# Optimization experiments

Hardware: AMD Instinct MI355X
Metric: run time of the kernel (lower is better)

Reference implementation:

```python
import jax, jax.numpy as jnp
import numpy as np

B = 2048      # batch
IN = 784      # input_dim (28*28, hardcoded by x.view(-1,28,28))
H = 512       # hidden_dim
OUT = 512     # output_dim
E = 8         # n_experts
ER = 4        # n_recurrent (experts 0..3 are LSTM experts)
ES = E - ER   # simple MLP experts
T = 28        # LSTM timesteps
F = 28        # LSTM input features per step
K = 5         # n_active = max(1, int(8*0.7))
TEMP = 2.718281828459045  # np.e


def setup_inputs() -> dict:
    key = jax.random.key(0)
    ks = jax.random.split(key, 14)
    s = 0.05
    return {
        "x":    jax.random.normal(ks[0], (B, IN), dtype=jnp.float32),
        # Boltzmann gate
        "Wg":   jax.random.normal(ks[1], (E, IN), dtype=jnp.float32) * s,
        "bg":   jnp.zeros((E,), dtype=jnp.float32),
        # Recurrent experts (stacked over ER): PyTorch LSTM layout, gate order i,f,g,o
        "Wih":  jax.random.normal(ks[2], (ER, 4 * H, F), dtype=jnp.float32) * s,
        "Whh":  jax.random.normal(ks[3], (ER, 4 * H, H), dtype=jnp.float32) * s,
        "bih":  jnp.zeros((ER, 4 * H), dtype=jnp.float32),
        "bhh":  jnp.zeros((ER, 4 * H), dtype=jnp.float32),
        "fcW":  jax.random.normal(ks[4], (ER, OUT, H), dtype=jnp.float32) * s,
        "fcb":  jnp.zeros((ER, OUT), dtype=jnp.float32),
        # Simple experts (stacked over ES)
        "W1":   jax.random.normal(ks[5], (ES, H, IN), dtype=jnp.float32) * s,
        "b1":   jnp.zeros((ES, H), dtype=jnp.float32),
        "W2":   jax.random.normal(ks[6], (ES, OUT, H), dtype=jnp.float32) * s,
        "b2":   jnp.zeros((ES, OUT), dtype=jnp.float32),
    }


def _forward(x, Wg, bg, Wih, Whh, bih, bhh, fcW, fcb, W1, b1, W2, b2):
    # --- Boltzmann gate: softmax(scores/T), top-k mask, renormalize ---
    scores = (x @ Wg.T + bg) / TEMP                    # [B,E]
    probs = jax.nn.softmax(scores, axis=-1)
    _, idx = jax.lax.top_k(probs, K)                   # [B,K]
    mask = jax.nn.one_hot(idx, E, dtype=probs.dtype).sum(axis=-2)  # [B,E]
    w = probs * mask
    weights = w / (w.sum(axis=-1, keepdims=True) + 1e-8)

    # --- Recurrent experts (vectorized over ER, scan over time) ---
    xs = x.reshape(B, T, F)
    xs_t = jnp.transpose(xs, (1, 0, 2))                # [T,B,F]

    def step(carry, x_t):
        h, c = carry                                   # each [ER,B,H]
        gates = (jnp.einsum('bi,egi->ebg', x_t, Wih) + bih[:, None, :]
                 + jnp.einsum('ebh,egh->ebg', h, Whh) + bhh[:, None, :])  # [ER,B,4H]
        i_g = jax.nn.sigmoid(gates[..., 0 * H:1 * H])
        f_g = jax.nn.sigmoid(gates[..., 1 * H:2 * H])
        g_g = jnp.tanh(gates[..., 2 * H:3 * H])
        o_g = jax.nn.sigmoid(gates[..., 3 * H:4 * H])
        c = f_g * c + i_g * g_g
        h = o_g * jnp.tanh(c)
        return (h, c), None

    h0 = jnp.zeros((ER, B, H), dtype=x.dtype)
    (h_last, _), _ = jax.lax.scan(step, (h0, h0), xs_t)
    rec_out = jnp.einsum('ebh,eoh->ebo', h_last, fcW) + fcb[:, None, :]   # [ER,B,OUT]

    # --- Simple experts (dropout is identity at eval) ---
    h1 = jax.nn.relu(jnp.einsum('bi,ehi->ebh', x, W1) + b1[:, None, :])   # [ES,B,H]
    simp_out = jnp.einsum('ebh,eoh->ebo', h1, W2) + b2[:, None, :]        # [ES,B,OUT]

    expert_outputs = jnp.concatenate([rec_out, simp_out], axis=0)         # [E,B,OUT]
    return jnp.einsum('be,ebo->bo', weights, expert_outputs)              # [B,OUT]


def reference(x, Wg, bg, Wih, Whh, bih, bhh, fcW, fcb, W1, b1, W2, b2):
    return _forward(x, Wg, bg, Wih, Whh, bih, bhh, fcW, fcb, W1, b1, W2, b2)
```

## Files before the change

### kernel.cpp

```cpp
#include <hip/hip_runtime.h>
#include <stdint.h>

#define CDIV(a,b) (((a)+(b)-1)/(b))

typedef unsigned short u16;
using bf16x8   = __attribute__((ext_vector_type(8))) short;
using floatx4  = __attribute__((ext_vector_type(4))) float;
using floatx16 = __attribute__((ext_vector_type(16))) float;

constexpr int B_N   = 2048;
constexpr int IN_N  = 784;
constexpr int H_N   = 512;
constexpr int OUT_N = 512;
constexpr int E_N   = 8;
constexpr int ER_N  = 4;
constexpr int ES_N  = 4;
constexpr int T_N   = 28;
constexpr int F_N   = 28;
constexpr int G4H   = 2048;
constexpr int KA    = 544;
constexpr int KB8   = KA / 8;
constexpr int NKI   = KA / 16;
constexpr int XP    = 800;

__device__ __forceinline__ u16 f2bf(float f) {
  union { float f; uint32_t u; } v; v.f = f;
  uint32_t r = v.u + 0x7fffu + ((v.u >> 16) & 1u);
  return (u16)(r >> 16);
}
__device__ __forceinline__ float sigm(float x) {
  return __builtin_amdgcn_rcpf(1.f + __expf(-x));
}
__device__ __forceinline__ float tanhf_(float x) {
  return __builtin_fmaf(-2.f, __builtin_amdgcn_rcpf(__expf(2.f * x) + 1.f), 1.f);
}

__device__ __forceinline__ void async16(const void* g, void* l) {
  __builtin_amdgcn_global_load_lds(
      (__attribute__((address_space(1))) void*)g,
      (__attribute__((address_space(3))) void*)l, 16, 0, 0);
}

__global__ __launch_bounds__(1024, 4)
void lstm_persist(const u16* __restrict__ Wc, const float* __restrict__ brec,
                  const u16* __restrict__ xb, u16* __restrict__ A0,
                  u16* __restrict__ A1, u16* __restrict__ Hlast,
                  int* __restrict__ Gbar)
{
  extern __shared__ __align__(16) u16 Ws[];
  const int tid  = threadIdx.x;
  const int lane = tid & 63;
  const int wave = tid >> 6;
  const int blk  = blockIdx.x;
  const int xcd  = blk & 7;
  const int i8   = blk >> 3;
  const int nt   = i8 & 15;
  const int g    = (i8 >> 4) * 8 + xcd;
  const int z    = g >> 2;
  const int mr   = g & 3;
  const int ln   = lane & 31;
  const int hw   = lane >> 5;
  const int gslot = g * 64;

  {
    const u16* Wsrc = Wc + (size_t)(z * 16 + nt) * (4 * KB8 * 256);
    for (int off = tid * 8; off < 4 * KB8 * 256; off += 1024 * 8)
      async16(Wsrc + off, Ws + off);
  }

  float bb[4];
#pragma unroll
  for (int j = 0; j < 4; ++j)
    bb[j] = brec[((z * 16 + nt) * 4 + j) * 32 + ln];

  float c[16];
#pragma unroll
  for (int r = 0; r < 16; ++r) c[r] = 0.f;

  const int mblk = mr * 16 + wave;
  const int hcol = nt * 32 + ln;
  const size_t zoff = (size_t)z * ((size_t)64 * KB8 * 256);
  __syncthreads();

  for (int t = 0; t < T_N; ++t) {
    const u16* Az  = ((t & 1) ? A1 : A0) + zoff;
    u16*       Aoz = ((t & 1) ? A0 : A1) + zoff;

    const u16* Ap = Az + ((size_t)mblk * KB8 + hw) * 256 + ln * 8;

    bf16x8 pa[2];
    pa[0] = *(const bf16x8*)Ap;
    pa[1] = *(const bf16x8*)(Ap + 512);

    floatx16 acc[4];
#pragma unroll
    for (int j = 0; j < 4; ++j)
#pragma unroll
      for (int r = 0; r < 16; ++r)
        acc[j][r] = bb[j];

#pragma unroll 2
    for (int kk = 0; kk < NKI; ++kk) {
      bf16x8 a = pa[kk & 1];
      if (kk + 2 < NKI)
        pa[kk & 1] = *(const bf16x8*)(Ap + (size_t)(kk + 2) * 512);
      const u16* Bp = Ws + (2 * kk + hw) * 256 + ln * 8;
      bf16x8 b0 = *(const bf16x8*)(Bp);
      bf16x8 b1 = *(const bf16x8*)(Bp + 1 * KB8 * 256);
      bf16x8 b2 = *(const bf16x8*)(Bp + 2 * KB8 * 256);
      bf16x8 b3 = *(const bf16x8*)(Bp + 3 * KB8 * 256);
      acc[0] = __builtin_amdgcn_mfma_f32_32x32x16_bf16(a, b0, acc[0], 0, 0, 0);
      acc[1] = __builtin_amdgcn_mfma_f32_32x32x16_bf16(a, b1, acc[1], 0, 0, 0);
      acc[2] = __builtin_amdgcn_mfma_f32_32x32x16_bf16(a, b2, acc[2], 0, 0, 0);
      acc[3] = __builtin_amdgcn_mfma_f32_32x32x16_bf16(a, b3, acc[3], 0, 0, 0);
    }

    const int last = (t == T_N - 1);
#pragma unroll
    for (int r = 0; r < 16; ++r) {
      float cv = sigm(acc[1][r]) * c[r] + sigm(acc[0][r]) * tanhf_(acc[2][r]);
      c[r] = cv;
      u16 hb = f2bf(sigm(acc[3][r]) * tanhf_(cv));
      int mrow = 4 * hw + (r & 3) + 8 * (r >> 2);
      if (!last)
        __builtin_nontemporal_store(hb,
            &Aoz[((size_t)mblk * KB8 + (hcol >> 3)) * 256 + mrow * 8 + (hcol & 7)]);
      else
        Hlast[((size_t)(z * B_N + mblk * 32 + mrow)) * H_N + hcol] = hb;
    }

    if (t + 1 < T_N) {
      for (int idx = nt * 1024 + tid; idx < 512 * F_N; idx += 16 * 1024) {
        int ml  = idx / F_N, col = idx - ml * F_N;
        int m   = mr * 512 + ml;
        int k   = H_N + col;
        __builtin_nontemporal_store(xb[(size_t)m * XP + (t + 1) * F_N + col],
            &Aoz[((size_t)(m >> 5) * KB8 + (k >> 3)) * 256 + (m & 31) * 8 + (k & 7)]);
      }

      __syncthreads();
      if (tid == 0) {
        __hip_atomic_fetch_add(&Gbar[gslot], 1, __ATOMIC_RELEASE,
                               __HIP_MEMORY_SCOPE_AGENT);
        const int target = 16 * (t + 1);
        while (__hip_atomic_load(&Gbar[gslot], __ATOMIC_RELAXED,
                                 __HIP_MEMORY_SCOPE_AGENT) < target)
          __builtin_amdgcn_s_sleep(1);
        __builtin_amdgcn_fence(__ATOMIC_ACQUIRE, "agent");
      }
      __syncthreads();
    }
  }
}

template<int RELU, int OBF>
__global__ __launch_bounds__(256, 2)
void gemm_bt(const u16* __restrict__ A, int lda, long sAz,
             const u16* __restrict__ Bw, int ldb, long sBz,
             const float* __restrict__ bias, int sBiz,
             void* __restrict__ Cv, int ldc, long sCz,
             int K)
{
  __shared__ __align__(16) u16 As[128 * 32];
  __shared__ __align__(16) u16 Bs[128 * 32];
  const int tid  = threadIdx.x;
  const int lane = tid & 63;
  const int wave = tid >> 6;
  const int m0 = blockIdx.y * 128;
  const int n0 = blockIdx.x * 128;
  const int z  = blockIdx.z;
  const u16* Ab = A  + (size_t)z * sAz;
  const u16* Bb = Bw + (size_t)z * sBz;

  const int wm   = (wave & 1) * 64;
  const int wn   = (wave >> 1) * 64;
  const int lm   = lane & 15;
  const int quad = lane >> 4;

  const int s0 = wave * 64 + lane;
  const int r0 = s0 >> 2, c0 = (s0 & 3) * 8;
  const int s1 = s0 + 256;
  const int r1 = s1 >> 2, c1 = (s1 & 3) * 8;

  floatx4 acc[4][4] = {};

  for (int k0 = 0; k0 < K; k0 += 32) {
    async16(Ab + (size_t)(m0 + r0) * lda + (k0 + c0), As + wave * 512);
    async16(Ab + (size_t)(m0 + r1) * lda + (k0 + c1), As + 2048 + wave * 512);
    async16(Bb + (size_t)(n0 + r0) * ldb + (k0 + c0), Bs + wave * 512);
    async16(Bb + (size_t)(n0 + r1) * ldb + (k0 + c1), Bs + 2048 + wave * 512);
    __syncthreads();
    bf16x8 af[4], bf_[4];
#pragma unroll
    for (int i = 0; i < 4; ++i)
      af[i] = *(const bf16x8*)&As[(wm + i * 16 + lm) * 32 + quad * 8];
#pragma unroll
    for (int j = 0; j < 4; ++j)
      bf_[j] = *(const bf16x8*)&Bs[(wn + j * 16 + lm) * 32 + quad * 8];
#pragma unroll
    for (int i = 0; i < 4; ++i)
#pragma unroll
      for (int j = 0; j < 4; ++j)
        acc[i][j] = __builtin_amdgcn_mfma_f32_16x16x32_bf16(af[i], bf_[j], acc[i][j], 0, 0, 0);
    __syncthreads();
  }

  float bj[4];
#pragma unroll
  for (int j = 0; j < 4; ++j)
    bj[j] = bias ? bias[z * sBiz + n0 + wn + j * 16 + lm] : 0.f;

#pragma unroll
  for (int i = 0; i < 4; ++i) {
#pragma unroll
    for (int r = 0; r < 4; ++r) {
      int m = m0 + wm + i * 16 + quad * 4 + r;
      size_t row = (size_t)z * sCz + (size_t)m * ldc;
#pragma unroll
      for (int j = 0; j < 4; ++j) {
        int n = n0 + wn + j * 16 + lm;
        float v = acc[i][j][r] + bj[j];
        if (RELU) v = fmaxf(v, 0.f);
        if (OBF) ((u16*)Cv)[row + n] = f2bf(v);
        else     ((float*)Cv)[row + n] = v;
      }
    }
  }
}

__global__ __launch_bounds__(256)
void gate_k(const float* __restrict__ x, const float* __restrict__ Wg,
            const float* __restrict__ bg, float* __restrict__ Wt)
{
  int lane = threadIdx.x & 63;
  int row  = blockIdx.x * 4 + (threadIdx.x >> 6);
  float ps[E_N];
#pragma unroll
  for (int e = 0; e < E_N; ++e) ps[e] = 0.f;
  const float* xr = x + (size_t)row * IN_N;
  for (int k = lane; k < IN_N; k += 64) {
    float xv = xr[k];
#pragma unroll
    for (int e = 0; e < E_N; ++e) ps[e] += xv * Wg[e * IN_N + k];
  }
#pragma unroll
  for (int e = 0; e < E_N; ++e) {
#pragma unroll
    for (int off = 32; off >= 1; off >>= 1) ps[e] += __shfl_down(ps[e], off);
  }
  if (lane == 0) {
    float s[E_N], mx = -1e30f;
#pragma unroll
    for (int e = 0; e < E_N; ++e) { s[e] = (ps[e] + bg[e]) * 0.36787944117144233f; mx = fmaxf(mx, s[e]); }
    float pr[E_N], sum = 0.f;
#pragma unroll
    for (int e = 0; e < E_N; ++e) { pr[e] = __expf(s[e] - mx); sum += pr[e]; }
    float inv = 1.f / sum;
#pragma unroll
    for (int e = 0; e < E_N; ++e) pr[e] *= inv;
    unsigned used = 0; float wsum = 0.f;
    for (int k = 0; k < 5; ++k) {
      int am = -1; float bv = -1.f;
      for (int e = 0; e < E_N; ++e)
        if (!((used >> e) & 1) && pr[e] > bv) { bv = pr[e]; am = e; }
      used |= 1u << am; wsum += pr[am];
    }
    float winv = 1.f / (wsum + 1e-8f);
    for (int e = 0; e < E_N; ++e)
      Wt[row * E_N + e] = ((used >> e) & 1) ? pr[e] * winv : 0.f;
  }
}

__global__ __launch_bounds__(256)
void combine_k(const float* __restrict__ O, const float* __restrict__ Wt, float* __restrict__ out)
{
  int idx = blockIdx.x * 256 + threadIdx.x;
  if (idx >= B_N * OUT_N) return;
  int b = idx / OUT_N;
  float a = 0.f;
#pragma unroll
  for (int e = 0; e < E_N; ++e)
    a += Wt[b * E_N + e] * O[(size_t)e * B_N * OUT_N + idx];
  out[idx] = a;
}

__global__ void prep_x_k(const float* __restrict__ x, u16* __restrict__ xb) {
  int idx = blockIdx.x * 256 + threadIdx.x;
  if (idx >= B_N * XP) return;
  int k = idx % XP, b = idx / XP;
  xb[idx] = f2bf(k < IN_N ? x[(size_t)b * IN_N + k] : 0.f);
}
__global__ void prep_wfrag_k(const float* __restrict__ Whh, const float* __restrict__ Wih,
                             u16* __restrict__ Wc) {
  int idx = blockIdx.x * 256 + threadIdx.x;
  if (idx >= ER_N * G4H * KA) return;
  int e8 = idx & 7, ln = (idx >> 3) & 31;
  int k8 = (idx >> 8) % KB8;
  int rest = (idx >> 8) / KB8;
  int j = rest & 3, nt = (rest >> 2) & 15, z = rest >> 6;
  int h = nt * 32 + ln, k = k8 * 8 + e8;
  int g = j * H_N + h;
  float v = 0.f;
  if (k < H_N)            v = Whh[((size_t)(z * G4H + g)) * H_N + k];
  else if (k < H_N + F_N) v = Wih[((size_t)(z * G4H + g)) * F_N + (k - H_N)];
  Wc[idx] = f2bf(v);
}
__global__ void prep_bfrag_k(const float* __restrict__ bih, const float* __restrict__ bhh,
                             float* __restrict__ o) {
  int idx = blockIdx.x * 256 + threadIdx.x;
  if (idx >= ER_N * G4H) return;
  int ln = idx & 31, j = (idx >> 5) & 3, nt = (idx >> 7) & 15, z = idx >> 11;
  int g = z * G4H + j * H_N + nt * 32 + ln;
  o[idx] = bih[g] + bhh[g];
}
__global__ void cvt_k(const float* __restrict__ in, u16* __restrict__ o, int n) {
  int idx = blockIdx.x * 256 + threadIdx.x;
  if (idx < n) o[idx] = f2bf(in[idx]);
}
__global__ void prep_w1_k(const float* __restrict__ W1, u16* __restrict__ o) {
  int idx = blockIdx.x * 256 + threadIdx.x;
  if (idx >= ES_N * H_N * XP) return;
  int k = idx % XP; int r = idx / XP;
  o[idx] = f2bf(k < IN_N ? W1[(size_t)r * IN_N + k] : 0.f);
}
__global__ void init_Afrag_k(u16* __restrict__ A0, u16* __restrict__ A1,
                             const u16* __restrict__ xb) {
  int idx = blockIdx.x * 256 + threadIdx.x;
  if (idx >= ER_N * B_N * KA) return;
  int e8 = idx & 7, mrow = (idx >> 3) & 31;
  int k8 = (idx >> 8) % KB8;
  int mb = ((idx >> 8) / KB8) & 63;
  int k = k8 * 8 + e8, m = mb * 32 + mrow;
  u16 v = 0;
  if (k >= H_N && k < H_N + F_N) v = xb[(size_t)m * XP + (k - H_N)];
  A0[idx] = v;
  A1[idx] = 0;
}
__global__ void zero_i_k(int* __restrict__ p, int n) {
  int i = blockIdx.x * 256 + threadIdx.x;
  if (i < n) p[i] = 0;
}

extern "C" void kernel_launch(void* const* d_in, const int* in_sizes, int n_in,
                              void* d_out, int out_size, void* d_ws, size_t ws_size,
                              hipStream_t stream) {
  const float* x   = (const float*)d_in[0];
  const float* Wg  = (const float*)d_in[1];
  const float* bg  = (const float*)d_in[2];
  const float* Wih = (const float*)d_in[3];
  const float* Whh = (const float*)d_in[4];
  const float* bih = (const float*)d_in[5];
  const float* bhh = (const float*)d_in[6];
  const float* fcW = (const float*)d_in[7];
  const float* fcb = (const float*)d_in[8];
  const float* W1  = (const float*)d_in[9];
  const float* b1  = (const float*)d_in[10];
  const float* W2  = (const float*)d_in[11];
  const float* b2  = (const float*)d_in[12];
  float* out = (float*)d_out;

  char* p = (char*)d_ws;
  auto take = [&](size_t bytes) { void* q = (void*)p; p += (bytes + 255) & ~(size_t)255; return q; };
  u16*   xb    = (u16*)  take((size_t)B_N * XP * 2);
  u16*   Wc    = (u16*)  take((size_t)ER_N * G4H * KA * 2);
  float* brec  = (float*)take((size_t)ER_N * G4H * 4);
  u16*   Wcomb = (u16*)  take((size_t)E_N * OUT_N * H_N * 2);
  u16*   W1b   = (u16*)  take((size_t)ES_N * H_N * XP * 2);
  u16*   A0    = (u16*)  take((size_t)ER_N * B_N * KA * 2);
  u16*   A1    = (u16*)  take((size_t)ER_N * B_N * KA * 2);
  u16*   Hcomb = (u16*)  take((size_t)E_N * B_N * H_N * 2);
  float* bcomb = (float*)take((size_t)E_N * OUT_N * 4);
  float* Ob    = (float*)take((size_t)E_N * B_N * OUT_N * 4);
  float* Wgt   = (float*)take((size_t)B_N * E_N * 4);
  int*   Gbar  = (int*)  take((size_t)16 * 64 * 4);

  u16* Hlast = Hcomb;
  u16* H1    = Hcomb + (size_t)ER_N * B_N * H_N;

  dim3 blk(256);
  prep_x_k    <<<CDIV(B_N * XP, 256),           blk, 0, stream>>>(x, xb);
  prep_wfrag_k<<<CDIV(ER_N * G4H * KA, 256),    blk, 0, stream>>>(Whh, Wih, Wc);
  prep_bfrag_k<<<CDIV(ER_N * G4H, 256),         blk, 0, stream>>>(bih, bhh, brec);
  cvt_k       <<<CDIV(ER_N * OUT_N * H_N, 256), blk, 0, stream>>>(fcW, Wcomb, ER_N * OUT_N * H_N);
  cvt_k       <<<CDIV(ES_N * OUT_N * H_N, 256), blk, 0, stream>>>(
      W2, Wcomb + (size_t)ER_N * OUT_N * H_N, ES_N * OUT_N * H_N);
  prep_w1_k   <<<CDIV(ES_N * H_N * XP, 256),    blk, 0, stream>>>(W1, W1b);
  init_Afrag_k<<<CDIV(ER_N * B_N * KA, 256),    blk, 0, stream>>>(A0, A1, xb);
  zero_i_k    <<<CDIV(16 * 64, 256),            blk, 0, stream>>>(Gbar, 16 * 64);
  gate_k      <<<B_N / 4,                       blk, 0, stream>>>(x, Wg, bg, Wgt);
  hipMemcpyAsync(bcomb, fcb, (size_t)ER_N * OUT_N * 4,
                 hipMemcpyDeviceToDevice, stream);
  hipMemcpyAsync(bcomb + (size_t)ER_N * OUT_N, b2, (size_t)ES_N * OUT_N * 4,
                 hipMemcpyDeviceToDevice, stream);

  gemm_bt<1, 1><<<dim3(H_N / 128, B_N / 128, ES_N), blk, 0, stream>>>(
      xb, XP, 0L,
      W1b, XP, (long)H_N * XP,
      b1, H_N,
      (void*)H1, H_N, (long)B_N * H_N, XP);

  constexpr unsigned ldsBytes = 4u * KB8 * 256u * 2u;
  hipFuncSetAttribute((const void*)lstm_persist,
                      hipFuncAttributeMaxDynamicSharedMemorySize, ldsBytes);
  {
    const u16* a_Wc = Wc; const float* a_br = brec; const u16* a_xb = xb;
    u16* a_A0 = A0; u16* a_A1 = A1; u16* a_Hl = Hlast; int* a_gb = Gbar;
    void* args[] = {(void*)&a_Wc, (void*)&a_br, (void*)&a_xb,
                    (void*)&a_A0, (void*)&a_A1, (void*)&a_Hl, (void*)&a_gb};
    hipLaunchCooperativeKernel((const void*)lstm_persist, dim3(256), dim3(1024),
                               args, ldsBytes, stream);
  }

  gemm_bt<0, 0><<<dim3(OUT_N / 128, B_N / 128, E_N), blk, 0, stream>>>(
      Hcomb, H_N, (long)B_N * H_N,
      Wcomb, H_N, (long)OUT_N * H_N,
      bcomb, OUT_N,
      (void*)Ob, OUT_N, (long)B_N * OUT_N, H_N);

  combine_k<<<CDIV(B_N * OUT_N, 256), blk, 0, stream>>>(Ob, Wgt, out);
}
```

Baseline: 0.9997 ms.

## Retile persistent LSTM blocks to 16 hidden columns by 64 batch rows

```diff
diff --git a/kernel.cpp b/kernel.cpp
--- a/kernel.cpp
+++ b/kernel.cpp
@@ -42,7 +42,7 @@
 }
 
 __global__ __launch_bounds__(1024, 4)
-void lstm_persist(const u16* __restrict__ Wc, const float* __restrict__ brec,
+void lstm_persist(const u16* __restrict__ Wc, const float* __restrict__ bq,
                   const u16* __restrict__ xb, u16* __restrict__ A0,
                   u16* __restrict__ A1, u16* __restrict__ Hlast,
                   int* __restrict__ Gbar)
@@ -52,33 +52,31 @@
   const int lane = tid & 63;
   const int wave = tid >> 6;
   const int blk  = blockIdx.x;
-  const int xcd  = blk & 7;
-  const int i8   = blk >> 3;
-  const int nt   = i8 & 15;
-  const int g    = (i8 >> 4) * 8 + xcd;
-  const int z    = g >> 2;
-  const int mr   = g & 3;
+  const int g    = blk & 7;
+  const int ntt  = blk >> 3;
+  const int z    = g >> 1;
+  const int mr   = g & 1;
   const int ln   = lane & 31;
   const int hw   = lane >> 5;
+  const bool lo  = (ln < 16);
   const int gslot = g * 64;
 
   {
-    const u16* Wsrc = Wc + (size_t)(z * 16 + nt) * (4 * KB8 * 256);
-    for (int off = tid * 8; off < 4 * KB8 * 256; off += 1024 * 8)
+    const u16* Wsrc = Wc + (size_t)(z * 32 + ntt) * (2 * KB8 * 256);
+    for (int off = tid * 8; off < 2 * KB8 * 256; off += 1024 * 8)
       async16(Wsrc + off, Ws + off);
   }
 
-  float bb[4];
-#pragma unroll
-  for (int j = 0; j < 4; ++j)
-    bb[j] = brec[((z * 16 + nt) * 4 + j) * 32 + ln];
+  const int hcol = ntt * 16 + (ln & 15);
+  floatx4 bqv = ((const floatx4*)bq)[z * H_N + hcol];
+  const float bA = lo ? bqv[0] : bqv[1];
+  const float bB = lo ? bqv[2] : bqv[3];
 
   float c[16];
 #pragma unroll
   for (int r = 0; r < 16; ++r) c[r] = 0.f;
 
-  const int mblk = mr * 16 + wave;
-  const int hcol = nt * 32 + ln;
+  const int mblk0 = mr * 32 + wave * 2;
   const size_t zoff = (size_t)z * ((size_t)64 * KB8 * 256);
   __syncthreads();
 
@@ -86,53 +84,66 @@
     const u16* Az  = ((t & 1) ? A1 : A0) + zoff;
     u16*       Aoz = ((t & 1) ? A0 : A1) + zoff;
 
-    const u16* Ap = Az + ((size_t)mblk * KB8 + hw) * 256 + ln * 8;
-
-    bf16x8 pa[2];
-    pa[0] = *(const bf16x8*)Ap;
-    pa[1] = *(const bf16x8*)(Ap + 512);
-
-    floatx16 acc[4];
-#pragma unroll
-    for (int j = 0; j < 4; ++j)
-#pragma unroll
-      for (int r = 0; r < 16; ++r)
-        acc[j][r] = bb[j];
+    const u16* Ap0 = Az + ((size_t)mblk0 * KB8 + hw) * 256 + ln * 8;
+    const u16* Ap1 = Az + ((size_t)(mblk0 + 1) * KB8 + hw) * 256 + ln * 8;
+
+    bf16x8 pa0 = *(const bf16x8*)Ap0;
+    bf16x8 pa1 = *(const bf16x8*)Ap1;
+
+    floatx16 acc0[2], acc1[2];
+#pragma unroll
+    for (int r = 0; r < 16; ++r) {
+      acc0[0][r] = bA; acc0[1][r] = bB;
+      acc1[0][r] = bA; acc1[1][r] = bB;
+    }
 
 #pragma unroll 2
     for (int kk = 0; kk < NKI; ++kk) {
-      bf16x8 a = pa[kk & 1];
-      if (kk + 2 < NKI)
-        pa[kk & 1] = *(const bf16x8*)(Ap + (size_t)(kk + 2) * 512);
+      bf16x8 a0 = pa0, a1 = pa1;
+      if (kk + 1 < NKI) {
+        pa0 = *(const bf16x8*)(Ap0 + (size_t)(kk + 1) * 512);
+        pa1 = *(const bf16x8*)(Ap1 + (size_t)(kk + 1) * 512);
+      }
       const u16* Bp = Ws + (2 * kk + hw) * 256 + ln * 8;
       bf16x8 b0 = *(const bf16x8*)(Bp);
-      bf16x8 b1 = *(const bf16x8*)(Bp + 1 * KB8 * 256);
-      bf16x8 b2 = *(const bf16x8*)(Bp + 2 * KB8 * 256);
-      bf16x8 b3 = *(const bf16x8*)(Bp + 3 * KB8 * 256);
-      acc[0] = __builtin_amdgcn_mfma_f32_32x32x16_bf16(a, b0, acc[0], 0, 0, 0);
-      acc[1] = __builtin_amdgcn_mfma_f32_32x32x16_bf16(a, b1, acc[1], 0, 0, 0);
-      acc[2] = __builtin_amdgcn_mfma_f32_32x32x16_bf16(a, b2, acc[2], 0, 0, 0);
-      acc[3] = __builtin_amdgcn_mfma_f32_32x32x16_bf16(a, b3, acc[3], 0, 0, 0);
+      bf16x8 b1 = *(const bf16x8*)(Bp + KB8 * 256);
+      acc0[0] = __builtin_amdgcn_mfma_f32_32x32x16_bf16(a0, b0, acc0[0], 0, 0, 0);
+      acc0[1] = __builtin_amdgcn_mfma_f32_32x32x16_bf16(a0, b1, acc0[1], 0, 0, 0);
+      acc1[0] = __builtin_amdgcn_mfma_f32_32x32x16_bf16(a1, b0, acc1[0], 0, 0, 0);
+      acc1[1] = __builtin_amdgcn_mfma_f32_32x32x16_bf16(a1, b1, acc1[1], 0, 0, 0);
     }
 
     const int last = (t == T_N - 1);
+    const int mb   = lo ? mblk0 : (mblk0 + 1);
 #pragma unroll
     for (int r = 0; r < 16; ++r) {
-      float cv = sigm(acc[1][r]) * c[r] + sigm(acc[0][r]) * tanhf_(acc[2][r]);
+      float x00 = acc0[0][r];
+      float x01 = acc0[1][r];
+      float x10 = acc1[0][r];
+      float x11 = acc1[1][r];
+      float y00 = __shfl_xor(x00, 16);
+      float y01 = __shfl_xor(x01, 16);
+      float y10 = __shfl_xor(x10, 16);
+      float y11 = __shfl_xor(x11, 16);
+      float pi = lo ? x00 : y10;
+      float pf = lo ? y00 : x10;
+      float pg = lo ? x01 : y11;
+      float po = lo ? y01 : x11;
+      float cv = sigm(pf) * c[r] + sigm(pi) * tanhf_(pg);
       c[r] = cv;
-      u16 hb = f2bf(sigm(acc[3][r]) * tanhf_(cv));
+      u16 hb = f2bf(sigm(po) * tanhf_(cv));
       int mrow = 4 * hw + (r & 3) + 8 * (r >> 2);
       if (!last)
         __builtin_nontemporal_store(hb,
-            &Aoz[((size_t)mblk * KB8 + (hcol >> 3)) * 256 + mrow * 8 + (hcol & 7)]);
+            &Aoz[((size_t)mb * KB8 + (hcol >> 3)) * 256 + mrow * 8 + (hcol & 7)]);
       else
-        Hlast[((size_t)(z * B_N + mblk * 32 + mrow)) * H_N + hcol] = hb;
+        Hlast[((size_t)(z * B_N + mb * 32 + mrow)) * H_N + hcol] = hb;
     }
 
     if (t + 1 < T_N) {
-      for (int idx = nt * 1024 + tid; idx < 512 * F_N; idx += 16 * 1024) {
+      for (int idx = ntt * 1024 + tid; idx < 1024 * F_N; idx += 32 * 1024) {
         int ml  = idx / F_N, col = idx - ml * F_N;
-        int m   = mr * 512 + ml;
+        int m   = mr * 1024 + ml;
         int k   = H_N + col;
         __builtin_nontemporal_store(xb[(size_t)m * XP + (t + 1) * F_N + col],
             &Aoz[((size_t)(m >> 5) * KB8 + (k >> 3)) * 256 + (m & 31) * 8 + (k & 7)]);
@@ -142,7 +153,7 @@
       if (tid == 0) {
         __hip_atomic_fetch_add(&Gbar[gslot], 1, __ATOMIC_RELEASE,
                                __HIP_MEMORY_SCOPE_AGENT);
-        const int target = 16 * (t + 1);
+        const int target = 32 * (t + 1);
         while (__hip_atomic_load(&Gbar[gslot], __ATOMIC_RELAXED,
                                  __HIP_MEMORY_SCOPE_AGENT) < target)
           __builtin_amdgcn_s_sleep(1);
@@ -297,20 +308,23 @@
   int e8 = idx & 7, ln = (idx >> 3) & 31;
   int k8 = (idx >> 8) % KB8;
   int rest = (idx >> 8) / KB8;
-  int j = rest & 3, nt = (rest >> 2) & 15, z = rest >> 6;
-  int h = nt * 32 + ln, k = k8 * 8 + e8;
-  int g = j * H_N + h;
+  int j = rest & 1, sm = rest >> 1;
+  int z = sm >> 5, nt = sm & 31;
+  int gate = j * 2 + (ln >= 16 ? 1 : 0);
+  int h = nt * 16 + (ln & 15);
+  int k = k8 * 8 + e8;
+  int g = gate * H_N + h;
   float v = 0.f;
   if (k < H_N)            v = Whh[((size_t)(z * G4H + g)) * H_N + k];
   else if (k < H_N + F_N) v = Wih[((size_t)(z * G4H + g)) * F_N + (k - H_N)];
   Wc[idx] = f2bf(v);
 }
-__global__ void prep_bfrag_k(const float* __restrict__ bih, const float* __restrict__ bhh,
-                             float* __restrict__ o) {
-  int idx = blockIdx.x * 256 + threadIdx.x;
-  if (idx >= ER_N * G4H) return;
-  int ln = idx & 31, j = (idx >> 5) & 3, nt = (idx >> 7) & 15, z = idx >> 11;
-  int g = z * G4H + j * H_N + nt * 32 + ln;
+__global__ void prep_bq_k(const float* __restrict__ bih, const float* __restrict__ bhh,
+                          float* __restrict__ o) {
+  int idx = blockIdx.x * 256 + threadIdx.x;
+  if (idx >= ER_N * H_N * 4) return;
+  int gate = idx & 3, h = (idx >> 2) & (H_N - 1), z = idx >> 11;
+  int g = z * G4H + gate * H_N + h;
   o[idx] = bih[g] + bhh[g];
 }
 __global__ void cvt_k(const float* __restrict__ in, u16* __restrict__ o, int n) {
@@ -363,7 +377,7 @@
   auto take = [&](size_t bytes) { void* q = (void*)p; p += (bytes + 255) & ~(size_t)255; return q; };
   u16*   xb    = (u16*)  take((size_t)B_N * XP * 2);
   u16*   Wc    = (u16*)  take((size_t)ER_N * G4H * KA * 2);
-  float* brec  = (float*)take((size_t)ER_N * G4H * 4);
+  float* bq    = (float*)take((size_t)ER_N * H_N * 4 * 4);
   u16*   Wcomb = (u16*)  take((size_t)E_N * OUT_N * H_N * 2);
   u16*   W1b   = (u16*)  take((size_t)ES_N * H_N * XP * 2);
   u16*   A0    = (u16*)  take((size_t)ER_N * B_N * KA * 2);
@@ -380,7 +394,7 @@
   dim3 blk(256);
   prep_x_k    <<<CDIV(B_N * XP, 256),           blk, 0, stream>>>(x, xb);
   prep_wfrag_k<<<CDIV(ER_N * G4H * KA, 256),    blk, 0, stream>>>(Whh, Wih, Wc);
-  prep_bfrag_k<<<CDIV(ER_N * G4H, 256),         blk, 0, stream>>>(bih, bhh, brec);
+  prep_bq_k   <<<CDIV(ER_N * H_N * 4, 256),     blk, 0, stream>>>(bih, bhh, bq);
   cvt_k       <<<CDIV(ER_N * OUT_N * H_N, 256), blk, 0, stream>>>(fcW, Wcomb, ER_N * OUT_N * H_N);
   cvt_k       <<<CDIV(ES_N * OUT_N * H_N, 256), blk, 0, stream>>>(
       W2, Wcomb + (size_t)ER_N * OUT_N * H_N, ES_N * OUT_N * H_N);
@@ -399,13 +413,13 @@
       b1, H_N,
       (void*)H1, H_N, (long)B_N * H_N, XP);
 
-  constexpr unsigned ldsBytes = 4u * KB8 * 256u * 2u;
+  constexpr unsigned ldsBytes = 2u * KB8 * 256u * 2u;
   hipFuncSetAttribute((const void*)lstm_persist,
                       hipFuncAttributeMaxDynamicSharedMemorySize, ldsBytes);
   {
-    const u16* a_Wc = Wc; const float* a_br = brec; const u16* a_xb = xb;
+    const u16* a_Wc = Wc; const float* a_bq = bq; const u16* a_xb = xb;
     u16* a_A0 = A0; u16* a_A1 = A1; u16* a_Hl = Hlast; int* a_gb = Gbar;
-    void* args[] = {(void*)&a_Wc, (void*)&a_br, (void*)&a_xb,
+    void* args[] = {(void*)&a_Wc, (void*)&a_bq, (void*)&a_xb,
                     (void*)&a_A0, (void*)&a_A1, (void*)&a_Hl, (void*)&a_gb};
     hipLaunchCooperativeKernel((const void*)lstm_persist, dim3(256), dim3(1024),
                                args, ldsBytes, stream);
```

Result: slower. 1.644 ms (+64.4%).
